# Optimization experiments

Hardware: AMD Instinct MI355X
Metric: run time of the kernel (lower is better)

The kernel has to match this reference:

```python
import jax, jax.numpy as jnp
import numpy as np

MASK_RATIO = 0.1


def _masked_channels(c, mask_ratio):
    # Faithful to the original: np.linspace float membership test against int i
    end = c * (1.0 - mask_ratio)
    stride = int(c * mask_ratio)
    mask = np.linspace(0.0, end, stride)
    sel = [i for i in range(c) if i in mask]
    return np.asarray(sel, dtype=np.int32)


def setup_inputs() -> dict:
    key = jax.random.key(0)
    input1 = jax.random.normal(key, (4, 100, 512, 512), dtype=jnp.float32)
    return {"input1": input1}


def reference(input1) -> jnp.ndarray:
    b, c, h, w = input1.shape
    sel = _masked_channels(c, MASK_RATIO)  # static channel index set
    x = input1.reshape(b, c, h * w)  # [N, L, D]
    # Original fills each selected channel with fresh torch.randn([N, D]);
    # one fused fill: noise [N, n_sel, D], single scatter over channel axis.
    noise = jax.random.normal(jax.random.key(1), (b, sel.shape[0], h * w), dtype=x.dtype)
    x = x.at[:, sel, :].set(noise)
    return x.reshape(b, c, h, w)
```

## Files before the change

### kernel.cpp

```cpp
#include <hip/hip_runtime.h>
#include <stdint.h>


typedef float f32x4 __attribute__((ext_vector_type(4)));

__device__ __forceinline__ uint32_t rotl32(uint32_t v, int r) {
    return (v << r) | (v >> (32 - r));
}

__device__ __forceinline__ void threefry2x32_key01(uint32_t x0, uint32_t x1,
                                                   uint32_t& o0, uint32_t& o1) {
    const uint32_t ks0 = 0u;
    const uint32_t ks1 = 1u;
    const uint32_t ks2 = 0x1BD11BDAu ^ ks0 ^ ks1;
    x0 += ks0; x1 += ks1;
#define TF_R(r) { x0 += x1; x1 = rotl32(x1, (r)); x1 ^= x0; }
    TF_R(13) TF_R(15) TF_R(26) TF_R(6)
    x0 += ks1; x1 += ks2 + 1u;
    TF_R(17) TF_R(29) TF_R(16) TF_R(24)
    x0 += ks2; x1 += ks0 + 2u;
    TF_R(13) TF_R(15) TF_R(26) TF_R(6)
    x0 += ks0; x1 += ks1 + 3u;
    TF_R(17) TF_R(29) TF_R(16) TF_R(24)
    x0 += ks1; x1 += ks2 + 4u;
    TF_R(13) TF_R(15) TF_R(26) TF_R(6)
    x0 += ks2; x1 += ks0 + 5u;
#undef TF_R
    o0 = x0; o1 = x1;
}

__device__ __forceinline__ float erfinv_xla_f32(float x) {
    float w = -log1pf(-x * x);
    float p;
    if (w < 5.0f) {
        w = w - 2.5f;
        p = 2.81022636e-08f;
        p = fmaf(p, w, 3.43273939e-07f);
        p = fmaf(p, w, -3.5233877e-06f);
        p = fmaf(p, w, -4.39150654e-06f);
        p = fmaf(p, w, 0.00021858087f);
        p = fmaf(p, w, -0.00125372503f);
        p = fmaf(p, w, -0.00417768164f);
        p = fmaf(p, w, 0.246640727f);
        p = fmaf(p, w, 1.50140941f);
    } else {
        w = sqrtf(w) - 3.0f;
        p = -0.000200214257f;
        p = fmaf(p, w, 0.000100950558f);
        p = fmaf(p, w, 0.00134934322f);
        p = fmaf(p, w, -0.00367342844f);
        p = fmaf(p, w, 0.00573950773f);
        p = fmaf(p, w, -0.0076224613f);
        p = fmaf(p, w, 0.00943887047f);
        p = fmaf(p, w, 1.00167406f);
        p = fmaf(p, w, 2.83297682f);
    }
    return p * x;
}

__device__ __forceinline__ float bits_to_normal(uint32_t bits) {
    float f = __uint_as_float((bits >> 9) | 0x3F800000u) - 1.0f;
    const float lo = __uint_as_float(0xBF7FFFFFu);
    float u = f * 2.0f + lo;
    u = fmaxf(lo, u);
    const float sqrt2 = __uint_as_float(0x3FB504F3u);
    return sqrt2 * erfinv_xla_f32(u);
}

constexpr uint32_t TILE_SHIFT = 11;
constexpr uint32_t TILES_PER_CH = 32;
constexpr uint32_t NBLOCKS = 400u * TILES_PER_CH;

__global__ __launch_bounds__(256) void random_masking_kernel(
        const f32x4* __restrict__ in, f32x4* __restrict__ out) {
    const uint32_t bid  = blockIdx.x;
    const uint32_t cb   = bid >> 5;
    const uint32_t tile = bid & (TILES_PER_CH - 1);
    const uint32_t c    = cb % 100u;
    const uint32_t base = (cb << 16) + (tile << TILE_SHIFT) + threadIdx.x;

    if (c % 10u != 0u) {
        f32x4 v[8];
#pragma unroll
        for (int k = 0; k < 8; ++k)
            v[k] = __builtin_nontemporal_load(in + base + k * 256);
#pragma unroll
        for (int k = 0; k < 8; ++k)
            __builtin_nontemporal_store(v[k], out + base + k * 256);
    } else {
        const uint32_t b = cb / 100u;
        const uint32_t s = c / 10u;
        const uint32_t jch = (b * 10u + s) << 18;
        const uint32_t fch = (tile << TILE_SHIFT) + threadIdx.x;
#pragma unroll
        for (int k = 0; k < 8; ++k) {
            const uint32_t j = jch + ((fch + k * 256) << 2);
            f32x4 o;
#pragma unroll
            for (int e = 0; e < 4; ++e) {
                uint32_t y0, y1;
                threefry2x32_key01(0u, j + (uint32_t)e, y0, y1);
                o[e] = bits_to_normal(y0 ^ y1);
            }
            __builtin_nontemporal_store(o, out + base + k * 256);
        }
    }
}

extern "C" void kernel_launch(void* const* d_in, const int* in_sizes, int n_in,
                              void* d_out, int out_size, void* d_ws, size_t ws_size,
                              hipStream_t stream) {
    const f32x4* in = reinterpret_cast<const f32x4*>(d_in[0]);
    f32x4* out = reinterpret_cast<f32x4*>(d_out);
    random_masking_kernel<<<NBLOCKS, 256, 0, stream>>>(in, out);
}
```

Baseline: 151.5 us.

## Merge noise and copy channels per block with double-buffered loads

Each block now handles a group of ten channels for one tile. It generates the noise channel while the first copy channel's loads are in flight, then streams the remaining nine channels through a two-slot register buffer, prefetching the next channel before storing the current one. The goal is to hide load latency behind the threefry/erfinv compute and remove the warp-level imbalance between copy blocks and noise blocks. The cost is a tenfold drop in block count, from 12800 to 1280, which may reduce occupancy and memory-level parallelism on a 256-CU part, along with higher register pressure.

```diff
diff --git a/kernel.cpp b/kernel.cpp
--- a/kernel.cpp
+++ b/kernel.cpp
@@ -67,34 +67,28 @@
     return sqrt2 * erfinv_xla_f32(u);
 }
 
-constexpr uint32_t TILE_SHIFT = 11;
-constexpr uint32_t TILES_PER_CH = 32;
-constexpr uint32_t NBLOCKS = 400u * TILES_PER_CH;
+constexpr uint32_t NBLOCKS = 40u * 32u;
 
 __global__ __launch_bounds__(256) void random_masking_kernel(
         const f32x4* __restrict__ in, f32x4* __restrict__ out) {
     const uint32_t bid  = blockIdx.x;
-    const uint32_t cb   = bid >> 5;
-    const uint32_t tile = bid & (TILES_PER_CH - 1);
-    const uint32_t c    = cb % 100u;
-    const uint32_t base = (cb << 16) + (tile << TILE_SHIFT) + threadIdx.x;
+    const uint32_t grp  = bid >> 5;
+    const uint32_t tile = bid & 31u;
+    const uint32_t cb0  = grp * 10u;
+    const uint32_t off  = (tile << 11) + threadIdx.x;
 
-    if (c % 10u != 0u) {
-        f32x4 v[8];
+    f32x4 buf[2][8];
 #pragma unroll
-        for (int k = 0; k < 8; ++k)
-            v[k] = __builtin_nontemporal_load(in + base + k * 256);
-#pragma unroll
-        for (int k = 0; k < 8; ++k)
-            __builtin_nontemporal_store(v[k], out + base + k * 256);
-    } else {
-        const uint32_t b = cb / 100u;
-        const uint32_t s = c / 10u;
+    for (int k = 0; k < 8; ++k)
+        buf[1][k] = __builtin_nontemporal_load(in + ((cb0 + 1) << 16) + off + k * 256);
+
+    {
+        const uint32_t b = cb0 / 100u;
+        const uint32_t s = (cb0 % 100u) / 10u;
         const uint32_t jch = (b * 10u + s) << 18;
-        const uint32_t fch = (tile << TILE_SHIFT) + threadIdx.x;
 #pragma unroll
         for (int k = 0; k < 8; ++k) {
-            const uint32_t j = jch + ((fch + k * 256) << 2);
+            const uint32_t j = jch + ((off + k * 256u) << 2);
             f32x4 o;
 #pragma unroll
             for (int e = 0; e < 4; ++e) {
@@ -102,8 +96,22 @@
                 threefry2x32_key01(0u, j + (uint32_t)e, y0, y1);
                 o[e] = bits_to_normal(y0 ^ y1);
             }
-            __builtin_nontemporal_store(o, out + base + k * 256);
+            __builtin_nontemporal_store(o, out + (cb0 << 16) + off + k * 256);
         }
+    }
+
+#pragma unroll
+    for (int ch = 1; ch <= 9; ++ch) {
+        if (ch < 9) {
+#pragma unroll
+            for (int k = 0; k < 8; ++k)
+                buf[(ch + 1) & 1][k] =
+                    __builtin_nontemporal_load(in + ((cb0 + ch + 1) << 16) + off + k * 256);
+        }
+#pragma unroll
+        for (int k = 0; k < 8; ++k)
+            __builtin_nontemporal_store(buf[ch & 1][k],
+                                        out + ((cb0 + ch) << 16) + off + k * 256);
     }
 }
 
```

Result: slower. 158.9 us (+4.9%).

## Interleave noise generation with copy traffic in grouped channel blocks

Applied to the files above, without the earlier changes.

Each block now covers one tile across a group of ten channels instead of one tile of one channel. It copies the nine unmasked channels in a loop and, inside each copy iteration, computes one vector of the masked channel's noise. The aim is to hide the ALU-heavy threefry/erfinv work behind memory loads, so noise blocks do not sit as a compute-bound tail. The grid shrinks to 1280 blocks with a launch-bounds occupancy hint of 5. The fewer, longer blocks may cut parallelism and make the tail less even.

```diff
diff --git a/kernel.cpp b/kernel.cpp
--- a/kernel.cpp
+++ b/kernel.cpp
@@ -67,34 +67,30 @@
     return sqrt2 * erfinv_xla_f32(u);
 }
 
-constexpr uint32_t TILE_SHIFT = 11;
-constexpr uint32_t TILES_PER_CH = 32;
-constexpr uint32_t NBLOCKS = 400u * TILES_PER_CH;
+constexpr uint32_t NBLOCKS = 40u * 32u;
 
-__global__ __launch_bounds__(256) void random_masking_kernel(
+__global__ __launch_bounds__(256, 5) void random_masking_kernel(
         const f32x4* __restrict__ in, f32x4* __restrict__ out) {
-    const uint32_t bid  = blockIdx.x;
-    const uint32_t cb   = bid >> 5;
-    const uint32_t tile = bid & (TILES_PER_CH - 1);
-    const uint32_t c    = cb % 100u;
-    const uint32_t base = (cb << 16) + (tile << TILE_SHIFT) + threadIdx.x;
+    const uint32_t bid   = blockIdx.x;
+    const uint32_t grp   = bid >> 5;
+    const uint32_t tile  = bid & 31u;
+    const uint32_t cb0   = grp * 10u;
+    const uint32_t off   = (tile << 11) + threadIdx.x;
+    const uint32_t jch   = grp << 18;
+    const uint32_t base0 = (cb0 << 16) + off;
 
-    if (c % 10u != 0u) {
+    for (uint32_t ch = 1; ch <= 9; ++ch) {
+        const f32x4* src = in  + base0 + (ch << 16);
+        f32x4*       dst = out + base0 + (ch << 16);
+
         f32x4 v[8];
 #pragma unroll
         for (int k = 0; k < 8; ++k)
-            v[k] = __builtin_nontemporal_load(in + base + k * 256);
-#pragma unroll
-        for (int k = 0; k < 8; ++k)
-            __builtin_nontemporal_store(v[k], out + base + k * 256);
-    } else {
-        const uint32_t b = cb / 100u;
-        const uint32_t s = c / 10u;
-        const uint32_t jch = (b * 10u + s) << 18;
-        const uint32_t fch = (tile << TILE_SHIFT) + threadIdx.x;
-#pragma unroll
-        for (int k = 0; k < 8; ++k) {
-            const uint32_t j = jch + ((fch + k * 256) << 2);
+            v[k] = __builtin_nontemporal_load(src + k * 256);
+
+        if (ch <= 8) {
+            const uint32_t q = ch - 1;
+            const uint32_t j = jch + ((off + q * 256u) << 2);
             f32x4 o;
 #pragma unroll
             for (int e = 0; e < 4; ++e) {
@@ -102,8 +98,12 @@
                 threefry2x32_key01(0u, j + (uint32_t)e, y0, y1);
                 o[e] = bits_to_normal(y0 ^ y1);
             }
-            __builtin_nontemporal_store(o, out + base + k * 256);
+            __builtin_nontemporal_store(o, out + base0 + q * 256);
         }
+
+#pragma unroll
+        for (int k = 0; k < 8; ++k)
+            __builtin_nontemporal_store(v[k], dst + k * 256);
     }
 }
 
```

Result: no change. 152.6 us, median of 2 (+0.8%).

## Split fused masking kernel into separate noise-generation and copy kernels

Applied to the files above, without the earlier changes.

Replaces the single kernel that branched per block between copying a channel and generating threefry normal noise with two launches. A noise kernel writes only the 40 masked channels, with 4 vectors per thread over 2560 blocks, and a copy kernel streams only the 360 unmasked channels. This removes the mix of compute-heavy and memory-bound blocks in one grid, which caused load imbalance and tail effects, and lets each kernel have a uniform profile. The cost is an extra launch and the loss of overlap between compute-bound noise work and the memory-bound copy within a single grid.

```diff
diff --git a/kernel.cpp b/kernel.cpp
--- a/kernel.cpp
+++ b/kernel.cpp
@@ -67,44 +67,45 @@
     return sqrt2 * erfinv_xla_f32(u);
 }
 
-constexpr uint32_t TILE_SHIFT = 11;
-constexpr uint32_t TILES_PER_CH = 32;
-constexpr uint32_t NBLOCKS = 400u * TILES_PER_CH;
+constexpr uint32_t NBLK_B = 2560;
 
-__global__ __launch_bounds__(256) void random_masking_kernel(
+__global__ __launch_bounds__(256) void noise_kernel(f32x4* __restrict__ out) {
+    const uint32_t tbase = (blockIdx.x << 10) + threadIdx.x;
+#pragma unroll
+    for (int k = 0; k < 4; ++k) {
+        const uint32_t idx  = tbase + k * 256;
+        const uint32_t grp  = idx >> 16;
+        const uint32_t off4 = idx & 65535u;
+        const uint32_t j    = (grp << 18) | (off4 << 2);
+        f32x4 o;
+#pragma unroll
+        for (int e = 0; e < 4; ++e) {
+            uint32_t y0, y1;
+            threefry2x32_key01(0u, j + (uint32_t)e, y0, y1);
+            o[e] = bits_to_normal(y0 ^ y1);
+        }
+        __builtin_nontemporal_store(o, out + (grp * 10u << 16) + off4);
+    }
+}
+
+constexpr uint32_t NBLK_A = 360u * 32u;
+
+__global__ __launch_bounds__(256) void copy_kernel(
         const f32x4* __restrict__ in, f32x4* __restrict__ out) {
     const uint32_t bid  = blockIdx.x;
-    const uint32_t cb   = bid >> 5;
-    const uint32_t tile = bid & (TILES_PER_CH - 1);
-    const uint32_t c    = cb % 100u;
-    const uint32_t base = (cb << 16) + (tile << TILE_SHIFT) + threadIdx.x;
+    const uint32_t cc   = bid >> 5;
+    const uint32_t tile = bid & 31u;
+    const uint32_t g    = cc / 9u;
+    const uint32_t cb   = g * 10u + (cc - g * 9u) + 1u;
+    const uint32_t base = (cb << 16) + (tile << 11) + threadIdx.x;
 
-    if (c % 10u != 0u) {
-        f32x4 v[8];
+    f32x4 v[8];
 #pragma unroll
-        for (int k = 0; k < 8; ++k)
-            v[k] = __builtin_nontemporal_load(in + base + k * 256);
+    for (int k = 0; k < 8; ++k)
+        v[k] = __builtin_nontemporal_load(in + base + k * 256);
 #pragma unroll
-        for (int k = 0; k < 8; ++k)
-            __builtin_nontemporal_store(v[k], out + base + k * 256);
-    } else {
-        const uint32_t b = cb / 100u;
-        const uint32_t s = c / 10u;
-        const uint32_t jch = (b * 10u + s) << 18;
-        const uint32_t fch = (tile << TILE_SHIFT) + threadIdx.x;
-#pragma unroll
-        for (int k = 0; k < 8; ++k) {
-            const uint32_t j = jch + ((fch + k * 256) << 2);
-            f32x4 o;
-#pragma unroll
-            for (int e = 0; e < 4; ++e) {
-                uint32_t y0, y1;
-                threefry2x32_key01(0u, j + (uint32_t)e, y0, y1);
-                o[e] = bits_to_normal(y0 ^ y1);
-            }
-            __builtin_nontemporal_store(o, out + base + k * 256);
-        }
-    }
+    for (int k = 0; k < 8; ++k)
+        __builtin_nontemporal_store(v[k], out + base + k * 256);
 }
 
 extern "C" void kernel_launch(void* const* d_in, const int* in_sizes, int n_in,
@@ -112,5 +113,6 @@
                               hipStream_t stream) {
     const f32x4* in = reinterpret_cast<const f32x4*>(d_in[0]);
     f32x4* out = reinterpret_cast<f32x4*>(d_out);
-    random_masking_kernel<<<NBLOCKS, 256, 0, stream>>>(in, out);
+    noise_kernel<<<NBLK_B, 256, 0, stream>>>(out);
+    copy_kernel<<<NBLK_A, 256, 0, stream>>>(in, out);
 }
```

New measurement: 171.6 us. +13.3%, slower.
